# Kernel optimization log

Hardware: AMD Instinct MI355X
Metric: run time of the kernel (lower is better)

## Reference

```python
import jax, jax.numpy as jnp
import numpy as np

NUM_NODE = 50000
NUM_REL = 50
NUM_EDGE = 1_000_000
NUM_TRI = 2_000_000
HIDDEN = 64


def setup_inputs() -> dict:
    key = jax.random.key(0)
    ks = jax.random.split(key, 9)
    rel_emb = jax.random.normal(ks[0], (NUM_REL, HIDDEN), dtype=jnp.float32)
    W_msg = jax.random.normal(ks[1], (2 * HIDDEN, HIDDEN), dtype=jnp.float32) / np.sqrt(2 * HIDDEN)
    W_upd = jax.random.normal(ks[2], (2 * HIDDEN, HIDDEN), dtype=jnp.float32) / np.sqrt(2 * HIDDEN)
    src = jax.random.randint(ks[3], (NUM_EDGE,), 0, NUM_NODE, dtype=jnp.int64 if jax.config.jax_enable_x64 else jnp.int32)
    dst = jax.random.randint(ks[4], (NUM_EDGE,), 0, NUM_NODE, dtype=src.dtype)
    rel = jax.random.randint(ks[5], (NUM_EDGE,), 0, NUM_REL, dtype=src.dtype)
    edge_ab = jax.random.randint(ks[6], (NUM_TRI,), 0, NUM_EDGE, dtype=src.dtype)
    edge_bc = jax.random.randint(ks[7], (NUM_TRI,), 0, NUM_EDGE, dtype=src.dtype)
    edge_ac = jax.random.randint(ks[8], (NUM_TRI,), 0, NUM_EDGE, dtype=src.dtype)
    return {
        "rel_emb": rel_emb, "W_msg": W_msg, "W_upd": W_upd,
        "src": src, "dst": dst, "rel": rel,
        "edge_ab": edge_ab, "edge_bc": edge_bc, "edge_ac": edge_ac,
    }


def reference(rel_emb, W_msg, W_upd, src, dst, rel, edge_ab, edge_bc, edge_ac):
    # Per-edge hidden state from relation embedding: [E, D]
    h = rel_emb[rel]
    num_edge = h.shape[0]
    # Triangle message: combine the two body edges of each grounding. [T, 2D]
    pair = jnp.concatenate([h[edge_ab], h[edge_bc]], axis=-1)
    msg = jax.nn.relu(pair @ W_msg)  # [T, D]
    # Scatter-add messages onto the head edge (a,c): irregular, memory-bound.
    agg = jax.ops.segment_sum(msg, edge_ac, num_segments=num_edge)  # [E, D]
    # Edge update.
    out = jax.nn.relu(jnp.concatenate([h, agg], axis=-1) @ W_upd)  # [E, D]
    return out
```

## Files before the change

### kernel.cpp

```cpp
#include <hip/hip_runtime.h>

#define HIDDEN 64
#define NREL 50
#define NPAIR (NREL * NREL)
#define TILE 4096

__global__ void precompute_tables(const float* __restrict__ rel_emb,
                                  const float* __restrict__ W_msg,
                                  const float* __restrict__ W_upd,
                                  float* __restrict__ M2,
                                  float* __restrict__ Hc) {
    const int p = blockIdx.x;
    const int j = threadIdx.x;
    const int ra = p / NREL, rb = p % NREL;

    __shared__ float msg[HIDDEN];

    const float* ha = rel_emb + ra * HIDDEN;
    const float* hb = rel_emb + rb * HIDDEN;

    float acc = 0.f;
    #pragma unroll 8
    for (int i = 0; i < HIDDEN; ++i) acc += ha[i] * W_msg[i * HIDDEN + j];
    #pragma unroll 8
    for (int i = 0; i < HIDDEN; ++i) acc += hb[i] * W_msg[(HIDDEN + i) * HIDDEN + j];
    msg[j] = fmaxf(acc, 0.f);
    __syncthreads();

    float acc2 = 0.f;
    #pragma unroll 8
    for (int k = 0; k < HIDDEN; ++k) acc2 += msg[k] * W_upd[(HIDDEN + k) * HIDDEN + j];
    M2[p * HIDDEN + j] = acc2;

    if (p < NREL) {
        float acc3 = 0.f;
        #pragma unroll 8
        for (int i = 0; i < HIDDEN; ++i) acc3 += rel_emb[p * HIDDEN + i] * W_upd[i * HIDDEN + j];
        Hc[p * HIDDEN + j] = acc3;
    }
}

__global__ void histogram(const int* __restrict__ edge_ac,
                          int* __restrict__ counts, int num_tri) {
    int i = blockIdx.x * blockDim.x + threadIdx.x;
    const int stride = gridDim.x * blockDim.x;
    for (; i < num_tri; i += stride) atomicAdd(&counts[edge_ac[i]], 1);
}

__global__ void scan_reduce(const int* __restrict__ counts,
                            int* __restrict__ blocksums, int n) {
    __shared__ int sdata[256];
    const int base = blockIdx.x * TILE;
    int s = 0;
    #pragma unroll
    for (int k = 0; k < 16; ++k) {
        const int i = base + k * 256 + threadIdx.x;
        if (i < n) s += counts[i];
    }
    sdata[threadIdx.x] = s;
    __syncthreads();
    for (int off = 128; off > 0; off >>= 1) {
        if (threadIdx.x < off) sdata[threadIdx.x] += sdata[threadIdx.x + off];
        __syncthreads();
    }
    if (threadIdx.x == 0) blocksums[blockIdx.x] = sdata[0];
}

__global__ void scan_blocksums(int* __restrict__ blocksums, int nb,
                               int* __restrict__ offsets, int num_edge, int num_tri) {
    __shared__ int sdata[256];
    const int v = (threadIdx.x < nb) ? blocksums[threadIdx.x] : 0;
    sdata[threadIdx.x] = v;
    __syncthreads();
    for (int off = 1; off < 256; off <<= 1) {
        const int t = (threadIdx.x >= off) ? sdata[threadIdx.x - off] : 0;
        __syncthreads();
        sdata[threadIdx.x] += t;
        __syncthreads();
    }
    if (threadIdx.x < nb) blocksums[threadIdx.x] = sdata[threadIdx.x] - v;
    if (threadIdx.x == 0) offsets[num_edge] = num_tri;
}

__global__ void scan_tile(const int* __restrict__ counts,
                          const int* __restrict__ blocksums,
                          int* __restrict__ offsets,
                          int* __restrict__ cursor, int n) {
    __shared__ int sdata[256];
    const int base = blockIdx.x * TILE + threadIdx.x * 16;
    int c[16];
    int s = 0;
    #pragma unroll
    for (int k = 0; k < 16; ++k) {
        const int i = base + k;
        c[k] = (i < n) ? counts[i] : 0;
        s += c[k];
    }
    sdata[threadIdx.x] = s;
    __syncthreads();
    for (int off = 1; off < 256; off <<= 1) {
        const int t = (threadIdx.x >= off) ? sdata[threadIdx.x - off] : 0;
        __syncthreads();
        sdata[threadIdx.x] += t;
        __syncthreads();
    }
    int run = blocksums[blockIdx.x] + (sdata[threadIdx.x] - s);
    #pragma unroll
    for (int k = 0; k < 16; ++k) {
        const int i = base + k;
        if (i < n) {
            offsets[i] = run;
            cursor[i]  = run;
            run += c[k];
        }
    }
}

__global__ void scatter_pairs(const int* __restrict__ rel,
                              const int* __restrict__ edge_ab,
                              const int* __restrict__ edge_bc,
                              const int* __restrict__ edge_ac,
                              int* __restrict__ cursor,
                              unsigned short* __restrict__ sorted_p, int num_tri) {
    int i = blockIdx.x * blockDim.x + threadIdx.x;
    const int stride = gridDim.x * blockDim.x;
    for (; i < num_tri; i += stride) {
        const int p = rel[edge_ab[i]] * NREL + rel[edge_bc[i]];
        const int pos = atomicAdd(&cursor[edge_ac[i]], 1);
        sorted_p[pos] = (unsigned short)p;
    }
}

__global__ void accumulate(const int* __restrict__ rel,
                           const int* __restrict__ offsets,
                           const unsigned short* __restrict__ sorted_p,
                           const float* __restrict__ M2,
                           const float* __restrict__ Hc,
                           float* __restrict__ out, int num_edge) {
    const int sub = threadIdx.x >> 4;
    const int l   = threadIdx.x & 15;
    int e = blockIdx.x * 16 + sub;
    const int estride = gridDim.x * 16;
    for (; e < num_edge; e += estride) {
        const int beg = offsets[e];
        const int end = offsets[e + 1];
        float4 acc = make_float4(0.f, 0.f, 0.f, 0.f);
        for (int k = beg; k < end; ++k) {
            const int p = sorted_p[k];
            const float4 m = ((const float4*)(M2 + p * HIDDEN))[l];
            acc.x += m.x; acc.y += m.y; acc.z += m.z; acc.w += m.w;
        }
        const float4 h = ((const float4*)(Hc + rel[e] * HIDDEN))[l];
        float4 o;
        o.x = fmaxf(acc.x + h.x, 0.f);
        o.y = fmaxf(acc.y + h.y, 0.f);
        o.z = fmaxf(acc.z + h.z, 0.f);
        o.w = fmaxf(acc.w + h.w, 0.f);
        ((float4*)out)[(size_t)e * 16 + l] = o;
    }
}

__global__ void scatter_tri(const int* __restrict__ rel,
                            const int* __restrict__ edge_ab,
                            const int* __restrict__ edge_bc,
                            const int* __restrict__ edge_ac,
                            const float* __restrict__ M2,
                            float* __restrict__ out, int num_tri) {
    const int lane   = threadIdx.x & 63;
    const int wave   = (int)((blockIdx.x * blockDim.x + threadIdx.x) >> 6);
    const int nwaves = (int)((gridDim.x * blockDim.x) >> 6);
    for (int t = wave; t < num_tri; t += nwaves) {
        const int p = rel[edge_ab[t]] * NREL + rel[edge_bc[t]];
        const float v = M2[p * HIDDEN + lane];
        unsafeAtomicAdd(&out[(size_t)edge_ac[t] * HIDDEN + lane], v);
    }
}

__global__ void finalize(const int* __restrict__ rel,
                         const float* __restrict__ Hc,
                         float* __restrict__ out, int num_edge) {
    const int total = num_edge * (HIDDEN / 4);
    int i = blockIdx.x * blockDim.x + threadIdx.x;
    const int stride = gridDim.x * blockDim.x;
    for (; i < total; i += stride) {
        const int e = i >> 4;
        const int q = i & 15;
        float4 a = ((const float4*)out)[i];
        float4 h = ((const float4*)(Hc + rel[e] * HIDDEN))[q];
        float4 o;
        o.x = fmaxf(a.x + h.x, 0.f);
        o.y = fmaxf(a.y + h.y, 0.f);
        o.z = fmaxf(a.z + h.z, 0.f);
        o.w = fmaxf(a.w + h.w, 0.f);
        ((float4*)out)[i] = o;
    }
}

extern "C" void kernel_launch(void* const* d_in, const int* in_sizes, int n_in,
                              void* d_out, int out_size, void* d_ws, size_t ws_size,
                              hipStream_t stream) {
    const float* rel_emb = (const float*)d_in[0];
    const float* W_msg   = (const float*)d_in[1];
    const float* W_upd   = (const float*)d_in[2];
    const int* rel     = (const int*)d_in[5];
    const int* edge_ab = (const int*)d_in[6];
    const int* edge_bc = (const int*)d_in[7];
    const int* edge_ac = (const int*)d_in[8];
    float* out = (float*)d_out;

    const int num_edge = in_sizes[5];
    const int num_tri  = in_sizes[6];
    const int nb = (num_edge + TILE - 1) / TILE;

    char* ws = (char*)d_ws;
    size_t off = 0;
    auto alloc = [&](size_t bytes) { char* p = ws + off; off = (off + bytes + 255) & ~(size_t)255; return p; };
    float*          M2        = (float*)alloc((size_t)NPAIR * HIDDEN * 4);
    float*          Hc        = (float*)alloc((size_t)NREL * HIDDEN * 4);
    int*            counts    = (int*)alloc((size_t)num_edge * 4);
    int*            offsets   = (int*)alloc((size_t)(num_edge + 1) * 4);
    int*            cursor    = (int*)alloc((size_t)num_edge * 4);
    unsigned short* sorted_p  = (unsigned short*)alloc((size_t)num_tri * 2);
    int*            blocksums = (int*)alloc((size_t)nb * 4);
    const size_t required = off;

    precompute_tables<<<NPAIR, HIDDEN, 0, stream>>>(rel_emb, W_msg, W_upd, M2, Hc);

    if (ws_size >= required && nb <= 256) {
        hipMemsetAsync(counts, 0, (size_t)num_edge * 4, stream);
        histogram<<<1024, 256, 0, stream>>>(edge_ac, counts, num_tri);
        scan_reduce<<<nb, 256, 0, stream>>>(counts, blocksums, num_edge);
        scan_blocksums<<<1, 256, 0, stream>>>(blocksums, nb, offsets, num_edge, num_tri);
        scan_tile<<<nb, 256, 0, stream>>>(counts, blocksums, offsets, cursor, num_edge);
        scatter_pairs<<<2048, 256, 0, stream>>>(rel, edge_ab, edge_bc, edge_ac,
                                                cursor, sorted_p, num_tri);
        const int ablocks = (num_edge + 15) / 16;
        accumulate<<<ablocks, 256, 0, stream>>>(rel, offsets, sorted_p, M2, Hc, out, num_edge);
    } else {
        hipMemsetAsync(d_out, 0, (size_t)out_size * sizeof(float), stream);
        scatter_tri<<<8192, 256, 0, stream>>>(rel, edge_ab, edge_bc, edge_ac, M2, out, num_tri);
        const int total4 = num_edge * (HIDDEN / 4);
        int fin_blocks = (total4 + 255) / 256;
        if (fin_blocks > 65535 * 8) fin_blocks = 65535 * 8;
        finalize<<<fin_blocks, 256, 0, stream>>>(rel, Hc, out, num_edge);
    }
}
```

Measured before the change: 574.3 us.

## Capture per-triangle rank during histogram to replace second atomic scatter pass

The histogram kernel now also computes the relation-pair index and records each triangle's rank within its head-edge bucket, taken from the atomicAdd return value, packed into one 32-bit word. The later placement pass then uses offsets plus rank with no atomics, and the cursor array and its writes in the scan are dropped. This removes a second full round of contended atomics over 2M triangles, at the cost of an extra 8MB packed buffer written and read back. The accumulate loop is also unrolled by two with dual accumulators to overlap the M2 gathers.

```diff
diff --git a/kernel.cpp b/kernel.cpp
--- a/kernel.cpp
+++ b/kernel.cpp
@@ -40,11 +40,19 @@
     }
 }
 
-__global__ void histogram(const int* __restrict__ edge_ac,
-                          int* __restrict__ counts, int num_tri) {
+__global__ void hist_capture(const int* __restrict__ rel,
+                             const int* __restrict__ edge_ab,
+                             const int* __restrict__ edge_bc,
+                             const int* __restrict__ edge_ac,
+                             int* __restrict__ counts,
+                             unsigned int* __restrict__ packed, int num_tri) {
     int i = blockIdx.x * blockDim.x + threadIdx.x;
     const int stride = gridDim.x * blockDim.x;
-    for (; i < num_tri; i += stride) atomicAdd(&counts[edge_ac[i]], 1);
+    for (; i < num_tri; i += stride) {
+        const int p = rel[edge_ab[i]] * NREL + rel[edge_bc[i]];
+        const unsigned int r = (unsigned int)atomicAdd(&counts[edge_ac[i]], 1);
+        packed[i] = (r << 16) | (unsigned int)p;
+    }
 }
 
 __global__ void scan_reduce(const int* __restrict__ counts,
@@ -84,8 +92,7 @@
 
 __global__ void scan_tile(const int* __restrict__ counts,
                           const int* __restrict__ blocksums,
-                          int* __restrict__ offsets,
-                          int* __restrict__ cursor, int n) {
+                          int* __restrict__ offsets, int n) {
     __shared__ int sdata[256];
     const int base = blockIdx.x * TILE + threadIdx.x * 16;
     int c[16];
@@ -108,26 +115,20 @@
     #pragma unroll
     for (int k = 0; k < 16; ++k) {
         const int i = base + k;
-        if (i < n) {
-            offsets[i] = run;
-            cursor[i]  = run;
-            run += c[k];
-        }
-    }
-}
-
-__global__ void scatter_pairs(const int* __restrict__ rel,
-                              const int* __restrict__ edge_ab,
-                              const int* __restrict__ edge_bc,
-                              const int* __restrict__ edge_ac,
-                              int* __restrict__ cursor,
-                              unsigned short* __restrict__ sorted_p, int num_tri) {
+        if (i < n) { offsets[i] = run; run += c[k]; }
+    }
+}
+
+__global__ void place(const int* __restrict__ edge_ac,
+                      const unsigned int* __restrict__ packed,
+                      const int* __restrict__ offsets,
+                      unsigned short* __restrict__ sorted_p, int num_tri) {
     int i = blockIdx.x * blockDim.x + threadIdx.x;
     const int stride = gridDim.x * blockDim.x;
     for (; i < num_tri; i += stride) {
-        const int p = rel[edge_ab[i]] * NREL + rel[edge_bc[i]];
-        const int pos = atomicAdd(&cursor[edge_ac[i]], 1);
-        sorted_p[pos] = (unsigned short)p;
+        const unsigned int v = packed[i];
+        const int pos = offsets[edge_ac[i]] + (int)(v >> 16);
+        sorted_p[pos] = (unsigned short)(v & 0xFFFFu);
     }
 }
 
@@ -142,20 +143,31 @@
     int e = blockIdx.x * 16 + sub;
     const int estride = gridDim.x * 16;
     for (; e < num_edge; e += estride) {
-        const int beg = offsets[e];
+        int k = offsets[e];
         const int end = offsets[e + 1];
-        float4 acc = make_float4(0.f, 0.f, 0.f, 0.f);
-        for (int k = beg; k < end; ++k) {
-            const int p = sorted_p[k];
-            const float4 m = ((const float4*)(M2 + p * HIDDEN))[l];
-            acc.x += m.x; acc.y += m.y; acc.z += m.z; acc.w += m.w;
+        const int r = rel[e];
+        const float4 h = ((const float4*)(Hc + r * HIDDEN))[l];
+
+        float4 a0 = make_float4(0.f, 0.f, 0.f, 0.f);
+        float4 a1 = make_float4(0.f, 0.f, 0.f, 0.f);
+        for (; k + 2 <= end; k += 2) {
+            const int p0 = sorted_p[k];
+            const int p1 = sorted_p[k + 1];
+            const float4 m0 = ((const float4*)M2)[p0 * 16 + l];
+            const float4 m1 = ((const float4*)M2)[p1 * 16 + l];
+            a0.x += m0.x; a0.y += m0.y; a0.z += m0.z; a0.w += m0.w;
+            a1.x += m1.x; a1.y += m1.y; a1.z += m1.z; a1.w += m1.w;
         }
-        const float4 h = ((const float4*)(Hc + rel[e] * HIDDEN))[l];
+        if (k < end) {
+            const int p0 = sorted_p[k];
+            const float4 m0 = ((const float4*)M2)[p0 * 16 + l];
+            a0.x += m0.x; a0.y += m0.y; a0.z += m0.z; a0.w += m0.w;
+        }
         float4 o;
-        o.x = fmaxf(acc.x + h.x, 0.f);
-        o.y = fmaxf(acc.y + h.y, 0.f);
-        o.z = fmaxf(acc.z + h.z, 0.f);
-        o.w = fmaxf(acc.w + h.w, 0.f);
+        o.x = fmaxf(a0.x + a1.x + h.x, 0.f);
+        o.y = fmaxf(a0.y + a1.y + h.y, 0.f);
+        o.z = fmaxf(a0.z + a1.z + h.z, 0.f);
+        o.w = fmaxf(a0.w + a1.w + h.w, 0.f);
         ((float4*)out)[(size_t)e * 16 + l] = o;
     }
 }
@@ -219,7 +231,7 @@
     float*          Hc        = (float*)alloc((size_t)NREL * HIDDEN * 4);
     int*            counts    = (int*)alloc((size_t)num_edge * 4);
     int*            offsets   = (int*)alloc((size_t)(num_edge + 1) * 4);
-    int*            cursor    = (int*)alloc((size_t)num_edge * 4);
+    unsigned int*   packed    = (unsigned int*)alloc((size_t)num_tri * 4);
     unsigned short* sorted_p  = (unsigned short*)alloc((size_t)num_tri * 2);
     int*            blocksums = (int*)alloc((size_t)nb * 4);
     const size_t required = off;
@@ -228,12 +240,12 @@
 
     if (ws_size >= required && nb <= 256) {
         hipMemsetAsync(counts, 0, (size_t)num_edge * 4, stream);
-        histogram<<<1024, 256, 0, stream>>>(edge_ac, counts, num_tri);
+        hist_capture<<<2048, 256, 0, stream>>>(rel, edge_ab, edge_bc, edge_ac,
+                                               counts, packed, num_tri);
         scan_reduce<<<nb, 256, 0, stream>>>(counts, blocksums, num_edge);
         scan_blocksums<<<1, 256, 0, stream>>>(blocksums, nb, offsets, num_edge, num_tri);
-        scan_tile<<<nb, 256, 0, stream>>>(counts, blocksums, offsets, cursor, num_edge);
-        scatter_pairs<<<2048, 256, 0, stream>>>(rel, edge_ab, edge_bc, edge_ac,
-                                                cursor, sorted_p, num_tri);
+        scan_tile<<<nb, 256, 0, stream>>>(counts, blocksums, offsets, num_edge);
+        place<<<2048, 256, 0, stream>>>(edge_ac, packed, offsets, sorted_p, num_tri);
         const int ablocks = (num_edge + 15) / 16;
         accumulate<<<ablocks, 256, 0, stream>>>(rel, offsets, sorted_p, M2, Hc, out, num_edge);
     } else {
```

After: 481.1 us. 16.2% less time.
